# Optimization experiments

Measured on AMD Instinct MI355X. Metric: run time of the kernel, lower is better.

The kernel has to match this reference:

```python
import jax, jax.numpy as jnp
import numpy as np

B, S, D, H, K = 2, 2048, 1024, 16, 16


def setup_inputs() -> dict:
    key = jax.random.key(0)
    ks = jax.random.split(key, 8)
    s = 0.02
    def w(k, shape):
        return s * jax.random.normal(k, shape, jnp.float32)
    return {
        "x": jax.random.normal(ks[0], (B, S, D), jnp.float32),
        "Wq": w(ks[1], (D, D)), "bq": jnp.zeros((D,), jnp.float32),
        "Wk": w(ks[2], (D, D)), "bk": jnp.zeros((D,), jnp.float32),
        "Wv": w(ks[3], (D, D)), "bv": jnp.zeros((D,), jnp.float32),
        "Wo": w(ks[4], (D, D)), "bo": jnp.zeros((D,), jnp.float32),
        "Ws1": w(ks[5], (D, D // 2)), "bs1": jnp.zeros((D // 2,), jnp.float32),
        "Ws2": w(ks[6], (D // 2, 1)), "bs2": jnp.zeros((1,), jnp.float32),
    }


def reference(x, Wq, bq, Wk, bk, Wv, bv, Wo, bo, Ws1, bs1, Ws2, bs2):
    Bx, Sx, Dx = x.shape
    Dh = Dx // H
    # QKV projections -> [B, H, S, Dh]
    q = (x @ Wq + bq).reshape(Bx, Sx, H, Dh).transpose(0, 2, 1, 3)
    k = (x @ Wk + bk).reshape(Bx, Sx, H, Dh).transpose(0, 2, 1, 3)
    v = (x @ Wv + bv).reshape(Bx, Sx, H, Dh).transpose(0, 2, 1, 3)
    scores = jnp.einsum('bhqd,bhkd->bhqk', q, k) / np.float32(np.sqrt(Dh))
    # Lightning-indexer importance: [B, S]; identical across heads, so compute once.
    imp = jax.nn.sigmoid(jax.nn.relu(x @ Ws1 + bs1) @ Ws2 + bs2)[..., 0]
    _, idx = jax.lax.top_k(imp, K)  # [B, K]
    sel = jnp.zeros((Bx, Sx), bool).at[jnp.arange(Bx)[:, None], idx].set(True)
    # sparse mask: position (i, j) kept if row i OR column j is a top-k token
    m2 = sel[:, :, None] | sel[:, None, :]  # [B, S, S]
    masked = jnp.where(m2[:, None, :, :], scores, -jnp.inf)
    w = jax.nn.softmax(masked, axis=-1)
    att = jnp.einsum('bhqk,bhkd->bhqd', w, v).transpose(0, 2, 1, 3).reshape(Bx, Sx, Dx)
    return att @ Wo + bo
```

## Files before the change

### kernel.cpp

```cpp
#include <hip/hip_runtime.h>
#include <math.h>

constexpr int Bb = 2, Ss = 2048, Dd = 1024, Hh = 16, Kk = 16;
constexpr float DELTA = 0.02f;

typedef __bf16 bf16x8 __attribute__((ext_vector_type(8)));
typedef __bf16 bf16x4 __attribute__((ext_vector_type(4)));
typedef float  f32x4  __attribute__((ext_vector_type(4)));

__device__ __forceinline__ void gld_lds16(const void* g, void* l) {
    __builtin_amdgcn_global_load_lds(
        (const __attribute__((address_space(1))) unsigned int*)g,
        (__attribute__((address_space(3))) unsigned int*)l, 16, 0, 0);
}

__global__ void __launch_bounds__(512) gemm_qkv_ind(
    const __bf16* __restrict__ xb, const __bf16* __restrict__ WqkvT,
    const __bf16* __restrict__ W1Th,
    const float* __restrict__ bq, const float* __restrict__ bk,
    const float* __restrict__ bv,
    __bf16* __restrict__ qb, __bf16* __restrict__ kb, __bf16* __restrict__ vb,
    const float* __restrict__ bs1, const float* __restrict__ Ws2,
    float* __restrict__ imp)
{
    __shared__ __bf16 As[256 * 32];
    __shared__ __bf16 Bs[128 * 32];

    const int bid  = blockIdx.x;
    const int cb   = bid % 28;
    const int bm   = (bid / 28) * 256;
    const int t    = threadIdx.x;
    const int wave = t >> 6;
    const int lane = t & 63;
    const int fr   = lane & 15;
    const int fq   = lane >> 4;
    const int K    = Dd;
    const bool ind = (cb >= 24);

    const __bf16* BT = ind ? (W1Th + (size_t)(cb - 24) * 128 * 1024)
                           : (WqkvT + (size_t)cb * 128 * 1024);

    const int wm = (wave & 3) * 64;
    const int wn = (wave >> 2) * 64;

    f32x4 acc[4][4] = {};

    for (int k0 = 0; k0 < K; k0 += 32) {
        #pragma unroll
        for (int l = 0; l < 2; ++l) {
            int c = l * 512 + t;
            int row = c >> 2, seg = c & 3;
            gld_lds16(xb + (size_t)(bm + row) * K + k0 + seg * 8,
                      As + (size_t)(l * 512 + wave * 64) * 8);
        }
        {
            int row = t >> 2, seg = t & 3;
            gld_lds16(BT + (size_t)row * K + k0 + seg * 8,
                      Bs + (size_t)(wave * 64) * 8);
        }
        __syncthreads();

        bf16x8 af[4], bf[4];
        #pragma unroll
        for (int i = 0; i < 4; ++i)
            af[i] = *(const bf16x8*)(As + (wm + i * 16 + fr) * 32 + fq * 8);
        #pragma unroll
        for (int j = 0; j < 4; ++j)
            bf[j] = *(const bf16x8*)(Bs + (wn + j * 16 + fr) * 32 + fq * 8);
        #pragma unroll
        for (int i = 0; i < 4; ++i)
            #pragma unroll
            for (int j = 0; j < 4; ++j)
                acc[i][j] = __builtin_amdgcn_mfma_f32_16x16x32_bf16(af[i], bf[j], acc[i][j], 0, 0, 0);
        __syncthreads();
    }

    const int cr = (lane >> 4) * 4;
    const int cc = lane & 15;

    if (!ind) {
        const int zone = cb >> 3;
        const int cl0  = cb * 128 - zone * 1024;
        const float* bias = (zone == 0) ? bq : (zone == 1) ? bk : bv;
        __bf16*      C    = (zone == 0) ? qb : (zone == 1) ? kb : vb;
        #pragma unroll
        for (int j = 0; j < 4; ++j) {
            int col = cl0 + wn + j * 16 + cc;
            float bb = bias[col];
            #pragma unroll
            for (int i = 0; i < 4; ++i) {
                #pragma unroll
                for (int r = 0; r < 4; ++r)
                    C[(size_t)(bm + wm + i * 16 + cr + r) * Dd + col] =
                        (__bf16)(acc[i][j][r] + bb);
            }
        }
    } else {
        const int hc0 = (cb - 24) * 128;
        float bb[4], w2[4];
        #pragma unroll
        for (int j = 0; j < 4; ++j) {
            int col = hc0 + wn + j * 16 + cc;
            bb[j] = bs1[col];
            w2[j] = Ws2[col];
        }
        #pragma unroll
        for (int i = 0; i < 4; ++i) {
            #pragma unroll
            for (int r = 0; r < 4; ++r) {
                float vsum = 0.f;
                #pragma unroll
                for (int j = 0; j < 4; ++j)
                    vsum += fmaxf(acc[i][j][r] + bb[j], 0.f) * w2[j];
                #pragma unroll
                for (int off = 8; off > 0; off >>= 1)
                    vsum += __shfl_xor(vsum, off, 16);
                if (cc == 0)
                    atomicAdd(imp + (bm + wm + i * 16 + cr + r), vsum);
            }
        }
    }
}

__global__ void __launch_bounds__(256) gemm_out(
    const __bf16* __restrict__ A, const __bf16* __restrict__ BT,
    const float* __restrict__ bias, float* __restrict__ C, int M, int N, int K)
{
    __shared__ __bf16 As[64 * 64];
    __shared__ __bf16 Bs[128 * 64];

    const int t    = threadIdx.x;
    const int wave = t >> 6;
    const int lane = t & 63;
    const int bm   = blockIdx.y * 64;
    const int bn   = blockIdx.x * 128;
    const int wm   = (wave & 1) * 32;
    const int wn   = (wave >> 1) * 64;
    const int fr   = lane & 15;
    const int fq   = lane >> 4;

    f32x4 acc[2][4] = {};

    for (int k0 = 0; k0 < K; k0 += 64) {
        #pragma unroll
        for (int l = 0; l < 2; ++l) {
            int c = l * 256 + t;
            int row = c >> 3, seg = (c & 7) ^ (row & 7);
            gld_lds16(A + (size_t)(bm + row) * K + k0 + seg * 8,
                      As + (size_t)(l * 256 + wave * 64) * 8);
        }
        #pragma unroll
        for (int l = 0; l < 4; ++l) {
            int c = l * 256 + t;
            int row = c >> 3, seg = (c & 7) ^ (row & 7);
            gld_lds16(BT + (size_t)(bn + row) * K + k0 + seg * 8,
                      Bs + (size_t)(l * 256 + wave * 64) * 8);
        }
        __syncthreads();

        #pragma unroll
        for (int s = 0; s < 2; ++s) {
            bf16x8 af[2], bf[4];
            #pragma unroll
            for (int i = 0; i < 2; ++i) {
                int row = wm + i * 16 + fr;
                af[i] = *(const bf16x8*)(As + row * 64 + (((s * 4 + fq) ^ (row & 7)) * 8));
            }
            #pragma unroll
            for (int j = 0; j < 4; ++j) {
                int row = wn + j * 16 + fr;
                bf[j] = *(const bf16x8*)(Bs + row * 64 + (((s * 4 + fq) ^ (row & 7)) * 8));
            }
            #pragma unroll
            for (int i = 0; i < 2; ++i)
                #pragma unroll
                for (int j = 0; j < 4; ++j)
                    acc[i][j] = __builtin_amdgcn_mfma_f32_16x16x32_bf16(af[i], bf[j], acc[i][j], 0, 0, 0);
        }
        __syncthreads();
    }

    const int cr = (lane >> 4) * 4;
    const int cc = lane & 15;
    #pragma unroll
    for (int j = 0; j < 4; ++j) {
        int col = bn + wn + j * 16 + cc;
        float bb = bias[col];
        #pragma unroll
        for (int i = 0; i < 2; ++i) {
            #pragma unroll
            for (int r = 0; r < 4; ++r)
                C[(size_t)(bm + wm + i * 16 + cr + r) * N + col] = acc[i][j][r] + bb;
        }
    }
}

__global__ void __launch_bounds__(256) prep_kernel(
    const float* __restrict__ x, __bf16* __restrict__ xb,
    float* __restrict__ imp, float* __restrict__ oacc,
    float* __restrict__ lsum, float* __restrict__ hbuf,
    int* __restrict__ ccount,
    const float* __restrict__ W0, const float* __restrict__ W1,
    const float* __restrict__ W2, const float* __restrict__ W3,
    __bf16* __restrict__ WqkvT, __bf16* __restrict__ WoT,
    const float* __restrict__ Ws1, __bf16* __restrict__ Th)
{
    __shared__ float tile[32][33];
    const int bid = blockIdx.x;

    if (bid < 4096) {
        int i = bid * 256 + threadIdx.x;
        if (i < Bb * Ss) imp[i] = 0.f;
        if (i < Bb * Hh * Kk * 64) oacc[i] = 0.f;
        if (i < Bb * Hh * Kk) lsum[i] = 0.f;
        if (i < Bb * 64 * 512) hbuf[i] = 0.f;
        if (i < Bb) ccount[i] = 0;
        float4 v = ((const float4*)x)[i];
        bf16x4 h = { (__bf16)v.x, (__bf16)v.y, (__bf16)v.z, (__bf16)v.w };
        ((bf16x4*)xb)[i] = h;
        return;
    }

    int tid = bid - 4096;
    int z   = tid >> 10;
    int rem = tid & 1023;
    int n0  = (rem & 31) * 32;
    int k0  = (rem >> 5) * 32;
    int tx = threadIdx.x & 31, ty = threadIdx.x >> 5;

    if (z < 4) {
        const float* W = (z == 0) ? W0 : (z == 1) ? W1 : (z == 2) ? W2 : W3;
        __bf16*      T = (z < 3) ? (WqkvT + (size_t)z * 1024 * 1024) : WoT;
        #pragma unroll
        for (int i = 0; i < 32; i += 8)
            tile[ty + i][tx] = W[(size_t)(k0 + ty + i) * 1024 + n0 + tx];
        __syncthreads();
        #pragma unroll
        for (int i = 0; i < 32; i += 8)
            T[(size_t)(n0 + ty + i) * 1024 + k0 + tx] = (__bf16)tile[tx][ty + i];
    } else {
        if (n0 >= 512) return;
        #pragma unroll
        for (int i = 0; i < 32; i += 8)
            tile[ty + i][tx] = Ws1[(size_t)(k0 + ty + i) * 512 + n0 + tx];
        __syncthreads();
        #pragma unroll
        for (int i = 0; i < 32; i += 8)
            Th[(size_t)(n0 + ty + i) * 1024 + k0 + tx] = (__bf16)tile[tx][ty + i];
    }
}

__global__ void __launch_bounds__(1024) topk_cand(
    const float* __restrict__ imp, int* __restrict__ cand_idx,
    int* __restrict__ ccount)
{
    int b = blockIdx.x;
    int t = threadIdx.x;
    int wave = t >> 6, lane = t & 63;
    __shared__ float vals[Ss];
    __shared__ float sv[16];
    __shared__ int   si[16];
    __shared__ float thr_s;
    __shared__ int   cnt_s;

    vals[t]        = imp[b * Ss + t];
    vals[t + 1024] = imp[b * Ss + t + 1024];
    __syncthreads();

    for (int it = 0; it < Kk; ++it) {
        float v0 = vals[t], v1 = vals[t + 1024];
        float best = v0; int bidx = t;
        if (v1 > best) { best = v1; bidx = t + 1024; }
        #pragma unroll
        for (int off = 32; off > 0; off >>= 1) {
            float ov = __shfl_xor(best, off, 64);
            int   oi = __shfl_xor(bidx, off, 64);
            if (ov > best || (ov == best && oi < bidx)) { best = ov; bidx = oi; }
        }
        if (lane == 0) { sv[wave] = best; si[wave] = bidx; }
        __syncthreads();
        if (t == 0) {
            float bv = sv[0]; int br = si[0];
            #pragma unroll
            for (int w = 1; w < 16; ++w)
                if (sv[w] > bv || (sv[w] == bv && si[w] < br)) { bv = sv[w]; br = si[w]; }
            cand_idx[b * 64 + it] = br;
            vals[br] = -1e30f;
            if (it == Kk - 1) { thr_s = bv - DELTA; cnt_s = Kk; }
        }
        __syncthreads();
    }

    float thr = thr_s;
    if (vals[t] > thr) {
        int p = atomicAdd(&cnt_s, 1);
        if (p < 64) cand_idx[b * 64 + p] = t;
    }
    if (vals[t + 1024] > thr) {
        int p = atomicAdd(&cnt_s, 1);
        if (p < 64) cand_idx[b * 64 + p] = t + 1024;
    }
    __syncthreads();
    if (t == 0) ccount[b] = min(cnt_s, 64);
}

__global__ void __launch_bounds__(256) rescore_h(
    const float* __restrict__ x, const float* __restrict__ Ws1,
    const int* __restrict__ cand_idx, const int* __restrict__ ccount,
    float* __restrict__ hbuf)
{
    const int c = blockIdx.x, kc = blockIdx.y, b = blockIdx.z;
    if (c >= ccount[b]) return;
    const int row = cand_idx[b * 64 + c];
    const int t = threadIdx.x;
    const int k0 = kc * 64;

    __shared__ float xs[64];
    if (t < 16)
        ((float4*)xs)[t] = ((const float4*)(x + ((size_t)(b * Ss + row)) * Dd + k0))[t];
    __syncthreads();

    float a0 = 0.f, a1 = 0.f;
    const float* W = Ws1 + (size_t)k0 * 512;
    #pragma unroll 16
    for (int kk = 0; kk < 64; ++kk) {
        float xv = xs[kk];
        a0 = fmaf(xv, W[kk * 512 + t], a0);
        a1 = fmaf(xv, W[kk * 512 + t + 256], a1);
    }
    float* hb = hbuf + ((size_t)(b * 64 + c)) * 512;
    atomicAdd(hb + t, a0);
    atomicAdd(hb + t + 256, a1);
}

__global__ void __launch_bounds__(256) rescore_fin(
    const float* __restrict__ hbuf, const float* __restrict__ bs1,
    const float* __restrict__ Ws2, const int* __restrict__ ccount,
    float* __restrict__ candz)
{
    const int c = blockIdx.x, b = blockIdx.y;
    if (c >= ccount[b]) return;
    const int t = threadIdx.x;
    __shared__ float red[256];
    const float* hb = hbuf + ((size_t)(b * 64 + c)) * 512;
    float zp = fmaxf(hb[t] + bs1[t], 0.f) * Ws2[t]
             + fmaxf(hb[t + 256] + bs1[t + 256], 0.f) * Ws2[t + 256];
    red[t] = zp;
    __syncthreads();
    for (int off = 128; off > 0; off >>= 1) {
        if (t < off) red[t] += red[t + off];
        __syncthreads();
    }
    if (t == 0) candz[b * 64 + c] = red[0];
}

__global__ void __launch_bounds__(64) select_k(
    const float* __restrict__ candz, const int* __restrict__ cand_idx,
    const int* __restrict__ ccount, int* __restrict__ sel_idx)
{
    const int b = blockIdx.x, t = threadIdx.x;
    const int cnt = ccount[b];
    float val = (t < cnt) ? candz[b * 64 + t] : -1e30f;
    int   row = (t < cnt) ? cand_idx[b * 64 + t] : 0x7fffffff;

    for (int it = 0; it < Kk; ++it) {
        float bv = val; int br = row;
        #pragma unroll
        for (int off = 1; off < 64; off <<= 1) {
            float ov = __shfl_xor(bv, off, 64);
            int   orw = __shfl_xor(br, off, 64);
            if (ov > bv || (ov == bv && orw < br)) { bv = ov; br = orw; }
        }
        if (row == br) val = -1e30f;
        if (t == 0) sel_idx[b * Kk + it] = br;
    }
}

__global__ void __launch_bounds__(256) attn_sparse(
    const __bf16* __restrict__ q, const __bf16* __restrict__ k,
    const __bf16* __restrict__ v, const int* __restrict__ sel_idx,
    __bf16* __restrict__ att)
{
    const int b  = blockIdx.z;
    const int h  = blockIdx.y;
    const int q0 = blockIdx.x * 16;
    const int t  = threadIdx.x;

    __shared__ float KT[64][17];
    __shared__ float Vs[16][64];
    __shared__ float qsh[16][65];
    __shared__ float wsh[16][16];
    __shared__ int   sj[16];

    if (t < 16) sj[t] = sel_idx[b * Kk + t];
    __syncthreads();

    {
        int row = t >> 4, d0 = (t & 15) * 4;
        bf16x4 kv = *(const bf16x4*)(k + ((size_t)(b * Ss + sj[row])) * Dd + h * 64 + d0);
        bf16x4 vv = *(const bf16x4*)(v + ((size_t)(b * Ss + sj[row])) * Dd + h * 64 + d0);
        bf16x4 qv = *(const bf16x4*)(q + ((size_t)(b * Ss + q0 + row)) * Dd + h * 64 + d0);
        #pragma unroll
        for (int i = 0; i < 4; ++i) {
            KT[d0 + i][row]  = (float)kv[i];
            Vs[row][d0 + i]  = (float)vv[i];
            qsh[row][d0 + i] = (float)qv[i];
        }
    }
    __syncthreads();

    const int wave = t >> 6, lane = t & 63;
    const int ql = lane >> 4, j = lane & 15;
    const int qi = wave * 4 + ql;

    float s = 0.f;
    #pragma unroll
    for (int d = 0; d < 64; ++d) s = fmaf(qsh[qi][d], KT[d][j], s);
    s *= 0.125f;

    float m = s;
    #pragma unroll
    for (int off = 8; off > 0; off >>= 1) m = fmaxf(m, __shfl_xor(m, off, 16));
    float e = __expf(s - m);
    float sum = e;
    #pragma unroll
    for (int off = 8; off > 0; off >>= 1) sum += __shfl_xor(sum, off, 16);
    wsh[qi][j] = e / sum;

    #pragma unroll
    for (int q2 = 0; q2 < 4; ++q2) {
        int qq = wave * 4 + q2;
        float o = 0.f;
        #pragma unroll
        for (int jj = 0; jj < 16; ++jj)
            o = fmaf(wsh[qq][jj], Vs[jj][lane], o);
        att[((size_t)(b * Ss + q0 + qq)) * Dd + h * 64 + lane] = (__bf16)o;
    }
}

__global__ void __launch_bounds__(256) attn_dense_one(
    const __bf16* __restrict__ q, const __bf16* __restrict__ k,
    const __bf16* __restrict__ v, const int* __restrict__ sel_idx,
    float* __restrict__ lsum, float* __restrict__ oacc)
{
    const int b  = blockIdx.z, h = blockIdx.y, j0 = blockIdx.x * 64;
    const int t  = threadIdx.x;

    __shared__ float Ks[64][68];
    __shared__ float Qs[16][68];
    __shared__ float Es[16][80];

    #pragma unroll
    for (int l = 0; l < 2; ++l) {
        int c = t + 256 * l;
        int row = c >> 3, seg = c & 7;
        bf16x8 kv = *(const bf16x8*)(k + ((size_t)(b * Ss + j0 + row)) * Dd + h * 64 + seg * 8);
        #pragma unroll
        for (int e = 0; e < 8; ++e) Ks[row][seg * 8 + e] = (float)kv[e];
    }
    if (t < 128) {
        int row = t >> 3, seg = t & 7;
        int i = sel_idx[b * Kk + row];
        bf16x8 qv = *(const bf16x8*)(q + ((size_t)(b * Ss + i)) * Dd + h * 64 + seg * 8);
        #pragma unroll
        for (int e = 0; e < 8; ++e) Qs[row][seg * 8 + e] = (float)qv[e];
    }
    __syncthreads();

    const int qi = t >> 4, ks = t & 15;
    const int bhq = (b * Hh + h) * Kk + qi;
    float psum = 0.f;
    #pragma unroll
    for (int s8 = 0; s8 < 4; ++s8) {
        int j = ks + s8 * 16;
        float sdot = 0.f;
        #pragma unroll
        for (int d4 = 0; d4 < 16; ++d4) {
            float4 qv = *(const float4*)&Qs[qi][d4 * 4];
            float4 kv = *(const float4*)&Ks[j][d4 * 4];
            sdot += qv.x * kv.x + qv.y * kv.y + qv.z * kv.z + qv.w * kv.w;
        }
        float e = __expf(sdot * 0.125f);
        Es[qi][j] = e;
        psum += e;
    }
    #pragma unroll
    for (int off = 8; off > 0; off >>= 1) psum += __shfl_xor(psum, off, 16);
    if (ks == 0) atomicAdd(lsum + bhq, psum);
    __syncthreads();

    #pragma unroll
    for (int l = 0; l < 2; ++l) {
        int c = t + 256 * l;
        int row = c >> 3, seg = c & 7;
        bf16x8 vv = *(const bf16x8*)(v + ((size_t)(b * Ss + j0 + row)) * Dd + h * 64 + seg * 8);
        #pragma unroll
        for (int e = 0; e < 8; ++e) Ks[row][seg * 8 + e] = (float)vv[e];
    }
    __syncthreads();

    const int d = t & 63, qg = t >> 6;
    #pragma unroll
    for (int qq = 0; qq < 4; ++qq) {
        int qx = qg * 4 + qq;
        float o = 0.f;
        #pragma unroll 8
        for (int jj = 0; jj < 64; ++jj)
            o = fmaf(Es[qx][jj], Ks[jj][d], o);
        atomicAdd(oacc + (size_t)((b * Hh + h) * Kk + qx) * 64 + d, o);
    }
}

__global__ void __launch_bounds__(64) attn_dense_fin(
    const float* __restrict__ oacc, const float* __restrict__ lsum,
    const int* __restrict__ sel_idx, __bf16* __restrict__ att)
{
    int bid = blockIdx.x;
    int qi = bid & 15, h = (bid >> 4) & 15, b = bid >> 8;
    int bhq = (b * Hh + h) * Kk + qi;
    int i = sel_idx[b * Kk + qi];
    float val = oacc[(size_t)bhq * 64 + threadIdx.x] / lsum[bhq];
    att[((size_t)(b * Ss + i)) * Dd + h * 64 + threadIdx.x] = (__bf16)val;
}

extern "C" void kernel_launch(void* const* d_in, const int* in_sizes, int n_in,
                              void* d_out, int out_size, void* d_ws, size_t ws_size,
                              hipStream_t stream)
{
    const float* x   = (const float*)d_in[0];
    const float* Wq  = (const float*)d_in[1];
    const float* bq  = (const float*)d_in[2];
    const float* Wk  = (const float*)d_in[3];
    const float* bk  = (const float*)d_in[4];
    const float* Wv  = (const float*)d_in[5];
    const float* bv  = (const float*)d_in[6];
    const float* Wo  = (const float*)d_in[7];
    const float* bo  = (const float*)d_in[8];
    const float* Ws1 = (const float*)d_in[9];
    const float* bs1 = (const float*)d_in[10];
    const float* Ws2 = (const float*)d_in[11];
    float* out = (float*)d_out;

    const size_t MSD = (size_t)Bb * Ss * Dd;
    const int M = Bb * Ss;

    char* p = (char*)d_ws;
    __bf16* qb  = (__bf16*)p; p += MSD * sizeof(__bf16);
    __bf16* kb  = (__bf16*)p; p += MSD * sizeof(__bf16);
    __bf16* vb  = (__bf16*)p; p += MSD * sizeof(__bf16);
    __bf16* att = (__bf16*)p; p += MSD * sizeof(__bf16);
    __bf16* xb  = (__bf16*)p; p += MSD * sizeof(__bf16);
    __bf16* WqkvT = (__bf16*)p; p += (size_t)3 * Dd * Dd * sizeof(__bf16);
    __bf16* WoT   = (__bf16*)p; p += (size_t)Dd * Dd * sizeof(__bf16);
    __bf16* W1Th  = (__bf16*)p; p += (size_t)512 * Dd * sizeof(__bf16);
    float* imp  = (float*)p; p += (size_t)Bb * Ss * sizeof(float);
    int* sel_idx = (int*)p; p += (size_t)Bb * Kk * sizeof(int);
    float* oacc = (float*)p; p += (size_t)Bb * Hh * Kk * 64 * sizeof(float);
    float* lsum = (float*)p; p += (size_t)Bb * Hh * Kk * sizeof(float);
    float* hbuf = (float*)p; p += (size_t)Bb * 64 * 512 * sizeof(float);
    int* ccount   = (int*)p; p += Bb * sizeof(int);
    int* cand_idx = (int*)p; p += (size_t)Bb * 64 * sizeof(int);
    float* candz  = (float*)p; p += (size_t)Bb * 64 * sizeof(float);

    prep_kernel<<<dim3(4096 + 5120), 256, 0, stream>>>(
        x, xb, imp, oacc, lsum, hbuf, ccount,
        Wq, Wk, Wv, Wo, WqkvT, WoT, Ws1, W1Th);
    gemm_qkv_ind<<<dim3(448), 512, 0, stream>>>(
        xb, WqkvT, W1Th, bq, bk, bv, qb, kb, vb, bs1, Ws2, imp);
    topk_cand<<<dim3(Bb), 1024, 0, stream>>>(imp, cand_idx, ccount);
    rescore_h<<<dim3(64, 16, Bb), 256, 0, stream>>>(x, Ws1, cand_idx, ccount, hbuf);
    rescore_fin<<<dim3(64, Bb), 256, 0, stream>>>(hbuf, bs1, Ws2, ccount, candz);
    select_k<<<dim3(Bb), 64, 0, stream>>>(candz, cand_idx, ccount, sel_idx);
    attn_sparse<<<dim3(Ss / 16, Hh, Bb), 256, 0, stream>>>(qb, kb, vb, sel_idx, att);
    attn_dense_one<<<dim3(Ss / 64, Hh, Bb), 256, 0, stream>>>(qb, kb, vb, sel_idx, lsum, oacc);
    attn_dense_fin<<<dim3(Bb * Hh * Kk), 64, 0, stream>>>(oacc, lsum, sel_idx, att);
    gemm_out<<<dim3(8, 64), 256, 0, stream>>>(att, WoT, bo, out, M, Dd, Dd);
}
```

Before: 252.6 us.

## Double K-tile depth with XOR-swizzled LDS in QKV GEMM; merge attention kernels

The QKV/indexer GEMM now stages 64-wide K slices per iteration instead of 32, with an XOR swizzle on the 16-byte segments to avoid LDS bank conflicts. This halves the number of barrier pairs per tile. Separately, the sparse-row and dense-column attention kernels are merged into one launch that branches on blockIdx.x, so the two phases can run concurrently and one launch is saved. The cost is doubled LDS usage in the GEMM, which may lower occupancy, and a larger shared buffer in the merged attention kernel.

```diff
diff --git a/kernel.cpp b/kernel.cpp
--- a/kernel.cpp
+++ b/kernel.cpp
@@ -23,8 +23,8 @@
     const float* __restrict__ bs1, const float* __restrict__ Ws2,
     float* __restrict__ imp)
 {
-    __shared__ __bf16 As[256 * 32];
-    __shared__ __bf16 Bs[128 * 32];
+    __shared__ __bf16 As[256 * 64];
+    __shared__ __bf16 Bs[128 * 64];
 
     const int bid  = blockIdx.x;
     const int cb   = bid % 28;
@@ -45,33 +45,42 @@
 
     f32x4 acc[4][4] = {};
 
-    for (int k0 = 0; k0 < K; k0 += 32) {
+    for (int k0 = 0; k0 < K; k0 += 64) {
+        #pragma unroll
+        for (int l = 0; l < 4; ++l) {
+            int c = l * 512 + t;
+            int row = c >> 3, seg = (c & 7) ^ (row & 7);
+            gld_lds16(xb + (size_t)(bm + row) * K + k0 + seg * 8,
+                      As + (size_t)(l * 512 + wave * 64) * 8);
+        }
         #pragma unroll
         for (int l = 0; l < 2; ++l) {
             int c = l * 512 + t;
-            int row = c >> 2, seg = c & 3;
-            gld_lds16(xb + (size_t)(bm + row) * K + k0 + seg * 8,
-                      As + (size_t)(l * 512 + wave * 64) * 8);
-        }
-        {
-            int row = t >> 2, seg = t & 3;
+            int row = c >> 3, seg = (c & 7) ^ (row & 7);
             gld_lds16(BT + (size_t)row * K + k0 + seg * 8,
-                      Bs + (size_t)(wave * 64) * 8);
-        }
-        __syncthreads();
-
-        bf16x8 af[4], bf[4];
-        #pragma unroll
-        for (int i = 0; i < 4; ++i)
-            af[i] = *(const bf16x8*)(As + (wm + i * 16 + fr) * 32 + fq * 8);
-        #pragma unroll
-        for (int j = 0; j < 4; ++j)
-            bf[j] = *(const bf16x8*)(Bs + (wn + j * 16 + fr) * 32 + fq * 8);
-        #pragma unroll
-        for (int i = 0; i < 4; ++i)
-            #pragma unroll
-            for (int j = 0; j < 4; ++j)
-                acc[i][j] = __builtin_amdgcn_mfma_f32_16x16x32_bf16(af[i], bf[j], acc[i][j], 0, 0, 0);
+                      Bs + (size_t)(l * 512 + wave * 64) * 8);
+        }
+        __syncthreads();
+
+        #pragma unroll
+        for (int s = 0; s < 2; ++s) {
+            bf16x8 af[4], bf[4];
+            #pragma unroll
+            for (int i = 0; i < 4; ++i) {
+                int row = wm + i * 16 + fr;
+                af[i] = *(const bf16x8*)(As + row * 64 + (((s * 4 + fq) ^ (row & 7)) * 8));
+            }
+            #pragma unroll
+            for (int j = 0; j < 4; ++j) {
+                int row = wn + j * 16 + fr;
+                bf[j] = *(const bf16x8*)(Bs + row * 64 + (((s * 4 + fq) ^ (row & 7)) * 8));
+            }
+            #pragma unroll
+            for (int i = 0; i < 4; ++i)
+                #pragma unroll
+                for (int j = 0; j < 4; ++j)
+                    acc[i][j] = __builtin_amdgcn_mfma_f32_16x16x32_bf16(af[i], bf[j], acc[i][j], 0, 0, 0);
+        }
         __syncthreads();
     }
 
@@ -376,138 +385,133 @@
     }
 }
 
-__global__ void __launch_bounds__(256) attn_sparse(
+__global__ void __launch_bounds__(256) attn_all(
     const __bf16* __restrict__ q, const __bf16* __restrict__ k,
     const __bf16* __restrict__ v, const int* __restrict__ sel_idx,
-    __bf16* __restrict__ att)
-{
-    const int b  = blockIdx.z;
-    const int h  = blockIdx.y;
-    const int q0 = blockIdx.x * 16;
-    const int t  = threadIdx.x;
-
-    __shared__ float KT[64][17];
-    __shared__ float Vs[16][64];
-    __shared__ float qsh[16][65];
-    __shared__ float wsh[16][16];
-    __shared__ int   sj[16];
-
-    if (t < 16) sj[t] = sel_idx[b * Kk + t];
-    __syncthreads();
-
-    {
-        int row = t >> 4, d0 = (t & 15) * 4;
-        bf16x4 kv = *(const bf16x4*)(k + ((size_t)(b * Ss + sj[row])) * Dd + h * 64 + d0);
-        bf16x4 vv = *(const bf16x4*)(v + ((size_t)(b * Ss + sj[row])) * Dd + h * 64 + d0);
-        bf16x4 qv = *(const bf16x4*)(q + ((size_t)(b * Ss + q0 + row)) * Dd + h * 64 + d0);
-        #pragma unroll
-        for (int i = 0; i < 4; ++i) {
-            KT[d0 + i][row]  = (float)kv[i];
-            Vs[row][d0 + i]  = (float)vv[i];
-            qsh[row][d0 + i] = (float)qv[i];
-        }
-    }
-    __syncthreads();
-
-    const int wave = t >> 6, lane = t & 63;
-    const int ql = lane >> 4, j = lane & 15;
-    const int qi = wave * 4 + ql;
-
-    float s = 0.f;
-    #pragma unroll
-    for (int d = 0; d < 64; ++d) s = fmaf(qsh[qi][d], KT[d][j], s);
-    s *= 0.125f;
-
-    float m = s;
-    #pragma unroll
-    for (int off = 8; off > 0; off >>= 1) m = fmaxf(m, __shfl_xor(m, off, 16));
-    float e = __expf(s - m);
-    float sum = e;
-    #pragma unroll
-    for (int off = 8; off > 0; off >>= 1) sum += __shfl_xor(sum, off, 16);
-    wsh[qi][j] = e / sum;
-
-    #pragma unroll
-    for (int q2 = 0; q2 < 4; ++q2) {
-        int qq = wave * 4 + q2;
-        float o = 0.f;
-        #pragma unroll
-        for (int jj = 0; jj < 16; ++jj)
-            o = fmaf(wsh[qq][jj], Vs[jj][lane], o);
-        att[((size_t)(b * Ss + q0 + qq)) * Dd + h * 64 + lane] = (__bf16)o;
-    }
-}
-
-__global__ void __launch_bounds__(256) attn_dense_one(
-    const __bf16* __restrict__ q, const __bf16* __restrict__ k,
-    const __bf16* __restrict__ v, const int* __restrict__ sel_idx,
-    float* __restrict__ lsum, float* __restrict__ oacc)
-{
-    const int b  = blockIdx.z, h = blockIdx.y, j0 = blockIdx.x * 64;
-    const int t  = threadIdx.x;
-
-    __shared__ float Ks[64][68];
-    __shared__ float Qs[16][68];
-    __shared__ float Es[16][80];
-
-    #pragma unroll
-    for (int l = 0; l < 2; ++l) {
-        int c = t + 256 * l;
-        int row = c >> 3, seg = c & 7;
-        bf16x8 kv = *(const bf16x8*)(k + ((size_t)(b * Ss + j0 + row)) * Dd + h * 64 + seg * 8);
-        #pragma unroll
-        for (int e = 0; e < 8; ++e) Ks[row][seg * 8 + e] = (float)kv[e];
-    }
-    if (t < 128) {
-        int row = t >> 3, seg = t & 7;
-        int i = sel_idx[b * Kk + row];
-        bf16x8 qv = *(const bf16x8*)(q + ((size_t)(b * Ss + i)) * Dd + h * 64 + seg * 8);
-        #pragma unroll
-        for (int e = 0; e < 8; ++e) Qs[row][seg * 8 + e] = (float)qv[e];
-    }
-    __syncthreads();
-
-    const int qi = t >> 4, ks = t & 15;
-    const int bhq = (b * Hh + h) * Kk + qi;
-    float psum = 0.f;
-    #pragma unroll
-    for (int s8 = 0; s8 < 4; ++s8) {
-        int j = ks + s8 * 16;
-        float sdot = 0.f;
-        #pragma unroll
-        for (int d4 = 0; d4 < 16; ++d4) {
-            float4 qv = *(const float4*)&Qs[qi][d4 * 4];
-            float4 kv = *(const float4*)&Ks[j][d4 * 4];
-            sdot += qv.x * kv.x + qv.y * kv.y + qv.z * kv.z + qv.w * kv.w;
-        }
-        float e = __expf(sdot * 0.125f);
-        Es[qi][j] = e;
-        psum += e;
-    }
-    #pragma unroll
-    for (int off = 8; off > 0; off >>= 1) psum += __shfl_xor(psum, off, 16);
-    if (ks == 0) atomicAdd(lsum + bhq, psum);
-    __syncthreads();
-
-    #pragma unroll
-    for (int l = 0; l < 2; ++l) {
-        int c = t + 256 * l;
-        int row = c >> 3, seg = c & 7;
-        bf16x8 vv = *(const bf16x8*)(v + ((size_t)(b * Ss + j0 + row)) * Dd + h * 64 + seg * 8);
-        #pragma unroll
-        for (int e = 0; e < 8; ++e) Ks[row][seg * 8 + e] = (float)vv[e];
-    }
-    __syncthreads();
-
-    const int d = t & 63, qg = t >> 6;
-    #pragma unroll
-    for (int qq = 0; qq < 4; ++qq) {
-        int qx = qg * 4 + qq;
-        float o = 0.f;
-        #pragma unroll 8
-        for (int jj = 0; jj < 64; ++jj)
-            o = fmaf(Es[qx][jj], Ks[jj][d], o);
-        atomicAdd(oacc + (size_t)((b * Hh + h) * Kk + qx) * 64 + d, o);
+    __bf16* __restrict__ att, float* __restrict__ lsum,
+    float* __restrict__ oacc)
+{
+    __shared__ __align__(16) float sm[6720];
+    const int b = blockIdx.z, h = blockIdx.y;
+    const int t = threadIdx.x;
+
+    if (blockIdx.x < 128) {
+        float (*KT)[17]  = (float(*)[17])sm;
+        float (*Vs)[64]  = (float(*)[64])(sm + 1088);
+        float (*qsh)[65] = (float(*)[65])(sm + 2112);
+        float (*wsh)[16] = (float(*)[16])(sm + 3152);
+        int*  sj         = (int*)(sm + 3408);
+        const int q0 = blockIdx.x * 16;
+
+        if (t < 16) sj[t] = sel_idx[b * Kk + t];
+        __syncthreads();
+
+        {
+            int row = t >> 4, d0 = (t & 15) * 4;
+            bf16x4 kv = *(const bf16x4*)(k + ((size_t)(b * Ss + sj[row])) * Dd + h * 64 + d0);
+            bf16x4 vv = *(const bf16x4*)(v + ((size_t)(b * Ss + sj[row])) * Dd + h * 64 + d0);
+            bf16x4 qv = *(const bf16x4*)(q + ((size_t)(b * Ss + q0 + row)) * Dd + h * 64 + d0);
+            #pragma unroll
+            for (int i = 0; i < 4; ++i) {
+                KT[d0 + i][row]  = (float)kv[i];
+                Vs[row][d0 + i]  = (float)vv[i];
+                qsh[row][d0 + i] = (float)qv[i];
+            }
+        }
+        __syncthreads();
+
+        const int wave = t >> 6, lane = t & 63;
+        const int ql = lane >> 4, j = lane & 15;
+        const int qi = wave * 4 + ql;
+
+        float s = 0.f;
+        #pragma unroll
+        for (int d = 0; d < 64; ++d) s = fmaf(qsh[qi][d], KT[d][j], s);
+        s *= 0.125f;
+
+        float m = s;
+        #pragma unroll
+        for (int off = 8; off > 0; off >>= 1) m = fmaxf(m, __shfl_xor(m, off, 16));
+        float e = __expf(s - m);
+        float sum = e;
+        #pragma unroll
+        for (int off = 8; off > 0; off >>= 1) sum += __shfl_xor(sum, off, 16);
+        wsh[qi][j] = e / sum;
+
+        #pragma unroll
+        for (int q2 = 0; q2 < 4; ++q2) {
+            int qq = wave * 4 + q2;
+            float o = 0.f;
+            #pragma unroll
+            for (int jj = 0; jj < 16; ++jj)
+                o = fmaf(wsh[qq][jj], Vs[jj][lane], o);
+            att[((size_t)(b * Ss + q0 + qq)) * Dd + h * 64 + lane] = (__bf16)o;
+        }
+    } else {
+        float (*Ks)[68] = (float(*)[68])sm;
+        float (*Qs)[68] = (float(*)[68])(sm + 4352);
+        float (*Es)[80] = (float(*)[80])(sm + 5440);
+        const int j0 = (blockIdx.x - 128) * 64;
+
+        #pragma unroll
+        for (int l = 0; l < 2; ++l) {
+            int c = t + 256 * l;
+            int row = c >> 3, seg = c & 7;
+            bf16x8 kv = *(const bf16x8*)(k + ((size_t)(b * Ss + j0 + row)) * Dd + h * 64 + seg * 8);
+            #pragma unroll
+            for (int e = 0; e < 8; ++e) Ks[row][seg * 8 + e] = (float)kv[e];
+        }
+        if (t < 128) {
+            int row = t >> 3, seg = t & 7;
+            int i = sel_idx[b * Kk + row];
+            bf16x8 qv = *(const bf16x8*)(q + ((size_t)(b * Ss + i)) * Dd + h * 64 + seg * 8);
+            #pragma unroll
+            for (int e = 0; e < 8; ++e) Qs[row][seg * 8 + e] = (float)qv[e];
+        }
+        __syncthreads();
+
+        const int qi = t >> 4, ks = t & 15;
+        const int bhq = (b * Hh + h) * Kk + qi;
+        float psum = 0.f;
+        #pragma unroll
+        for (int s8 = 0; s8 < 4; ++s8) {
+            int j = ks + s8 * 16;
+            float sdot = 0.f;
+            #pragma unroll
+            for (int d4 = 0; d4 < 16; ++d4) {
+                float4 qv = *(const float4*)&Qs[qi][d4 * 4];
+                float4 kv = *(const float4*)&Ks[j][d4 * 4];
+                sdot += qv.x * kv.x + qv.y * kv.y + qv.z * kv.z + qv.w * kv.w;
+            }
+            float e = __expf(sdot * 0.125f);
+            Es[qi][j] = e;
+            psum += e;
+        }
+        #pragma unroll
+        for (int off = 8; off > 0; off >>= 1) psum += __shfl_xor(psum, off, 16);
+        if (ks == 0) atomicAdd(lsum + bhq, psum);
+        __syncthreads();
+
+        #pragma unroll
+        for (int l = 0; l < 2; ++l) {
+            int c = t + 256 * l;
+            int row = c >> 3, seg = c & 7;
+            bf16x8 vv = *(const bf16x8*)(v + ((size_t)(b * Ss + j0 + row)) * Dd + h * 64 + seg * 8);
+            #pragma unroll
+            for (int e = 0; e < 8; ++e) Ks[row][seg * 8 + e] = (float)vv[e];
+        }
+        __syncthreads();
+
+        const int d = t & 63, qg = t >> 6;
+        #pragma unroll
+        for (int qq = 0; qq < 4; ++qq) {
+            int qx = qg * 4 + qq;
+            float o = 0.f;
+            #pragma unroll 8
+            for (int jj = 0; jj < 64; ++jj)
+                o = fmaf(Es[qx][jj], Ks[jj][d], o);
+            atomicAdd(oacc + (size_t)((b * Hh + h) * Kk + qx) * 64 + d, o);
+        }
     }
 }
 
@@ -571,8 +575,8 @@
     rescore_h<<<dim3(64, 16, Bb), 256, 0, stream>>>(x, Ws1, cand_idx, ccount, hbuf);
     rescore_fin<<<dim3(64, Bb), 256, 0, stream>>>(hbuf, bs1, Ws2, ccount, candz);
     select_k<<<dim3(Bb), 64, 0, stream>>>(candz, cand_idx, ccount, sel_idx);
-    attn_sparse<<<dim3(Ss / 16, Hh, Bb), 256, 0, stream>>>(qb, kb, vb, sel_idx, att);
-    attn_dense_one<<<dim3(Ss / 64, Hh, Bb), 256, 0, stream>>>(qb, kb, vb, sel_idx, lsum, oacc);
+    attn_all<<<dim3(160, Hh, Bb), 256, 0, stream>>>(
+        qb, kb, vb, sel_idx, att, lsum, oacc);
     attn_dense_fin<<<dim3(Bb * Hh * Kk), 64, 0, stream>>>(oacc, lsum, sel_idx, att);
     gemm_out<<<dim3(8, 64), 256, 0, stream>>>(att, WoT, bo, out, M, Dd, Dd);
 }
```

Measured after the change: 243.0 us. 3.8% less time.
